# Kernel tuning notes

Hardware: AMD Instinct MI355X
Metric: run time of the kernel (lower is better)

## Reference

```python
import jax, jax.numpy as jnp
import numpy as np


def setup_inputs() -> dict:
    key0 = jax.random.key(0)
    kq, kk, kv = jax.random.split(key0, 3)
    B, S, E = 4, 2048, 1024
    query = jax.random.normal(kq, (B, S, E), dtype=jnp.float32)
    key = jax.random.normal(kk, (B, S, E), dtype=jnp.float32)
    value = jax.random.normal(kv, (B, S, E), dtype=jnp.float32)
    attn_mask = jnp.zeros((B, S, S), dtype=jnp.float32)
    return {"query": query, "key": key, "value": value, "attn_mask": attn_mask}


def reference(query, key, value, attn_mask):
    # qk = Q K^T / sqrt(E) + mask; softmax over last dim; dropout is
    # identity in eval mode (reference baseline); out = attn @ V.
    E = query.shape[-1]
    scale = 1.0 / jnp.sqrt(jnp.asarray(E, dtype=query.dtype))
    qk = jnp.einsum("bqe,bke->bqk", query, key) * scale + attn_mask
    attn = jax.nn.softmax(qk, axis=-1)
    out = jnp.einsum("bqk,bke->bqe", attn, value)
    return out
```

## Files before the change

### kernel.cpp

```cpp
#include <hip/hip_runtime.h>
#include <stdint.h>
#include <math.h>

typedef unsigned short u16;
typedef short bf16x8 __attribute__((ext_vector_type(8)));
typedef unsigned short u16x8 __attribute__((ext_vector_type(8)));
typedef unsigned short u16x4 __attribute__((ext_vector_type(4)));
typedef float f32x4 __attribute__((ext_vector_type(4)));

typedef __attribute__((address_space(1))) const void gvoid;
typedef __attribute__((address_space(3))) void lvoid;

#define LOG2E 1.4426950408889634f

__device__ __forceinline__ float bf2f(u16 u) {
  union { unsigned int i; float f; } v; v.i = ((unsigned int)u) << 16; return v.f;
}
__device__ __forceinline__ u16 f2bf(float f) {
  union { float ff; unsigned int i; } v; v.ff = f;
  unsigned int x = v.i;
  return (u16)((x + 0x7FFFu + ((x >> 16) & 1u)) >> 16);
}

__global__ __launch_bounds__(256)
void cvt2_f32_bf16(const float* __restrict__ s0, u16* __restrict__ d0,
                   const float* __restrict__ s1, u16* __restrict__ d1, long n)
{
  const long nb = n / 2048;
  const float* src = (blockIdx.x < nb) ? s0 : s1;
  u16* dst         = (blockIdx.x < nb) ? d0 : d1;
  const long bid   = (blockIdx.x < nb) ? blockIdx.x : (blockIdx.x - nb);
  long i = (bid * 256 + threadIdx.x) * 8;
  if (i + 8 > n) return;
  f32x4 a = *(const f32x4*)&src[i];
  f32x4 b = *(const f32x4*)&src[i + 4];
  u16x8 o;
#pragma unroll
  for (int j = 0; j < 4; j++) { o[j] = f2bf(a[j]); o[4 + j] = f2bf(b[j]); }
  *(u16x8*)&dst[i] = o;
}

__global__ __launch_bounds__(256)
void cvt_f32_bf16(const float* __restrict__ src, u16* __restrict__ dst, long n)
{
  long i = ((long)blockIdx.x * 256 + threadIdx.x) * 8;
  if (i + 8 > n) return;
  f32x4 a = *(const f32x4*)&src[i];
  f32x4 b = *(const f32x4*)&src[i + 4];
  u16x8 o;
#pragma unroll
  for (int j = 0; j < 4; j++) { o[j] = f2bf(a[j]); o[4 + j] = f2bf(b[j]); }
  *(u16x8*)&dst[i] = o;
}

__global__ __launch_bounds__(256)
void transcvt_v(const float* __restrict__ V, u16* __restrict__ VT, int S, int E)
{
  __shared__ u16 t[64][72];
  const int b = blockIdx.z;
  const float* Vb = V + (long)b * S * E;
  u16* VTb = VT + (long)b * S * E;
  const int k0 = blockIdx.x * 64, n0 = blockIdx.y * 64;
  const int tid = threadIdx.x;
#pragma unroll
  for (int p = 0; p < 2; p++) {
    int kk = p * 32 + (tid >> 3);
    int nn = (tid & 7) * 8;
    f32x4 a = *(const f32x4*)&Vb[(long)(k0 + kk) * E + n0 + nn];
    f32x4 c = *(const f32x4*)&Vb[(long)(k0 + kk) * E + n0 + nn + 4];
#pragma unroll
    for (int j = 0; j < 4; j++) { t[nn + j][kk] = f2bf(a[j]); t[nn + 4 + j][kk] = f2bf(c[j]); }
  }
  __syncthreads();
#pragma unroll
  for (int p = 0; p < 2; p++) {
    int nn = p * 32 + (tid >> 3);
    int kk = (tid & 7) * 8;
    u16x8 u;
#pragma unroll
    for (int j = 0; j < 8; j++) u[j] = t[nn][kk + j];
    *(u16x8*)&VTb[(long)(n0 + nn) * S + k0 + kk] = u;
  }
}

__global__ __launch_bounds__(512, 1)
void gemm_bt_256(const u16* __restrict__ A, int lda,
                 const u16* __restrict__ B, int ldb, long bBatchStride,
                 u16* __restrict__ C, int ldc,
                 int K, float scale, int S)
{
  __shared__ u16 LA[2][256][64];
  __shared__ u16 LB[2][256][64];

  const int tid  = threadIdx.x;
  const int lane = tid & 63;
  const int wave = tid >> 6;
  const int wm   = wave >> 2;
  const int wn   = wave & 3;
  const long gTile = (long)blockIdx.y * 256;
  const int  bidx  = (int)(gTile / S);
  const int  nTile = blockIdx.x * 256;

  const u16* Ab = A + gTile * (long)lda;
  const u16* Bb = B + (long)bidx * bBatchStride + (long)nTile * ldb;

  const int lm  = lane & 15;
  const int lkc = (lane >> 4) * 8;
  const int srw = lane >> 3;
  const int scg = (lane & 7) * 8;

  f32x4 acc[8][4];
#pragma unroll
  for (int i = 0; i < 8; i++)
#pragma unroll
    for (int j = 0; j < 4; j++) acc[i][j] = (f32x4){0.f, 0.f, 0.f, 0.f};

  bf16x8 afr[8], bA[4], bB[4];

#define STG_A(buf, T, h)                                                      \
  {                                                                           \
    _Pragma("unroll")                                                         \
    for (int p_ = 0; p_ < 2; p_++) {                                          \
      const int ch_ = wave * 2 + p_;                                          \
      const int rr_ = (h) * 128 + ch_ * 8 + srw;                              \
      __builtin_amdgcn_global_load_lds(                                       \
          (gvoid*)&Ab[(long)rr_ * lda + (T) * 64 + scg],                      \
          (lvoid*)((char*)&LA[0][0][0] + (buf) * 32768 + (h) * 16384 + ch_ * 1024), \
          16, 0, 0);                                                          \
    }                                                                         \
  }
#define STG_B(buf, T, h)                                                      \
  {                                                                           \
    _Pragma("unroll")                                                         \
    for (int p_ = 0; p_ < 2; p_++) {                                          \
      const int ch_ = wave * 2 + p_;                                          \
      const int rr_ = (h) * 128 + ch_ * 8 + srw;                              \
      __builtin_amdgcn_global_load_lds(                                       \
          (gvoid*)&Bb[(long)rr_ * ldb + (T) * 64 + scg],                      \
          (lvoid*)((char*)&LB[0][0][0] + (buf) * 32768 + (h) * 16384 + ch_ * 1024), \
          16, 0, 0);                                                          \
    }                                                                         \
  }

#define LDA_HALF(buf, mh)                                                     \
  {                                                                           \
    _Pragma("unroll")                                                         \
    for (int m_ = 0; m_ < 4; m_++)                                            \
      _Pragma("unroll")                                                       \
      for (int kk_ = 0; kk_ < 2; kk_++)                                       \
        afr[m_ * 2 + kk_] = *(const bf16x8*)&LA[buf][wm * 128 + ((mh) * 4 + m_) * 16 + lm][kk_ * 32 + lkc]; \
  }
#define LDB_HALF(buf, nh, dst)                                                \
  {                                                                           \
    _Pragma("unroll")                                                         \
    for (int n_ = 0; n_ < 2; n_++)                                            \
      _Pragma("unroll")                                                       \
      for (int kk_ = 0; kk_ < 2; kk_++)                                       \
        dst[n_ * 2 + kk_] = *(const bf16x8*)&LB[buf][wn * 64 + ((nh) * 2 + n_) * 16 + lm][kk_ * 32 + lkc]; \
  }

#define PH(mh, nh, bp)                                                        \
  {                                                                           \
    __builtin_amdgcn_sched_barrier(0);                                        \
    __builtin_amdgcn_s_barrier();                                             \
    asm volatile("s_waitcnt lgkmcnt(0)" ::: "memory");                        \
    __builtin_amdgcn_sched_barrier(0);                                        \
    __builtin_amdgcn_s_setprio(1);                                            \
    _Pragma("unroll")                                                         \
    for (int m_ = 0; m_ < 4; m_++)                                            \
      _Pragma("unroll")                                                       \
      for (int n_ = 0; n_ < 2; n_++)                                          \
        _Pragma("unroll")                                                     \
        for (int kk_ = 0; kk_ < 2; kk_++)                                     \
          acc[(mh) * 4 + m_][(nh) * 2 + n_] =                                 \
              __builtin_amdgcn_mfma_f32_16x16x32_bf16(                        \
                  afr[m_ * 2 + kk_], bp[n_ * 2 + kk_],                        \
                  acc[(mh) * 4 + m_][(nh) * 2 + n_], 0, 0, 0);                \
    __builtin_amdgcn_s_setprio(0);                                            \
    __builtin_amdgcn_sched_barrier(0);                                        \
    __builtin_amdgcn_s_barrier();                                             \
  }

  const int NT = K >> 6;
  const int NI = NT >> 1;

  STG_A(0, 0, 0); STG_A(0, 0, 1); STG_B(0, 0, 0); STG_B(0, 0, 1);
  STG_A(1, 1, 0); STG_B(1, 1, 0);
  asm volatile("s_waitcnt vmcnt(0)" ::: "memory");
  __builtin_amdgcn_sched_barrier(0);
  __builtin_amdgcn_s_barrier();

  for (int i = 0; i < NI - 1; i++) {
    const int t0 = 2 * i, t1 = t0 + 1;
    LDA_HALF(0, 0); LDB_HALF(0, 0, bA);
    STG_B(1, t1, 1);
    PH(0, 0, bA);
    LDB_HALF(0, 1, bB);
    STG_A(1, t1, 1);
    PH(0, 1, bB);
    LDA_HALF(0, 1);
    STG_A(0, t0 + 2, 0);
    PH(1, 0, bA);
    STG_B(0, t0 + 2, 0);
    asm volatile("s_waitcnt vmcnt(4)" ::: "memory");
    PH(1, 1, bB);
    LDA_HALF(1, 0); LDB_HALF(1, 0, bA);
    STG_B(0, t0 + 2, 1);
    PH(0, 0, bA);
    LDB_HALF(1, 1, bB);
    STG_A(0, t0 + 2, 1);
    PH(0, 1, bB);
    LDA_HALF(1, 1);
    STG_A(1, t1 + 2, 0);
    PH(1, 0, bA);
    STG_B(1, t1 + 2, 0);
    asm volatile("s_waitcnt vmcnt(4)" ::: "memory");
    PH(1, 1, bB);
  }

  {
    const int t1 = NT - 1;
    LDA_HALF(0, 0); LDB_HALF(0, 0, bA);
    STG_B(1, t1, 1);
    PH(0, 0, bA);
    LDB_HALF(0, 1, bB);
    STG_A(1, t1, 1);
    PH(0, 1, bB);
    LDA_HALF(0, 1);
    PH(1, 0, bA);
    asm volatile("s_waitcnt vmcnt(0)" ::: "memory");
    PH(1, 1, bB);
    LDA_HALF(1, 0); LDB_HALF(1, 0, bA);
    PH(0, 0, bA);
    LDB_HALF(1, 1, bB);
    PH(0, 1, bB);
    LDA_HALF(1, 1);
    PH(1, 0, bA);
    PH(1, 1, bB);
  }

  const int lr = (lane >> 4) * 4;
#pragma unroll
  for (int mf = 0; mf < 8; mf++) {
#pragma unroll
    for (int nf = 0; nf < 4; nf++) {
      long gr = gTile + wm * 128 + mf * 16 + lr;
      int  cc = nTile + wn * 64 + nf * 16 + lm;
#pragma unroll
      for (int i2 = 0; i2 < 4; i2++)
        C[(gr + i2) * (long)ldc + cc] = f2bf(acc[mf][nf][i2] * scale);
    }
  }
#undef STG_A
#undef STG_B
#undef LDA_HALF
#undef LDB_HALF
#undef PH
}

template<int HASMASK, int COUT>
__global__ __launch_bounds__(256, 3)
void gemm_bt_fast(const u16* __restrict__ A, int lda, long aRowOff,
                  const u16* __restrict__ B, int ldb, long bBatchStride,
                  void* __restrict__ Cp, int ldc, long cRowOff,
                  const float* __restrict__ maskf,
                  int K, float scale, long g0, int S)
{
  const int tid  = threadIdx.x;
  const int lane = tid & 63;
  const int wave = tid >> 6;
  const long gTile = g0 + (long)blockIdx.y * 128;
  const int  bidx  = (int)(gTile / S);
  const int  nTile = blockIdx.x * 128;

  __shared__ u16 As[128][32];
  __shared__ u16 Bs[128][32];

  const u16* Ab = A + (gTile - aRowOff) * (long)lda;
  const u16* Bb = B + (long)bidx * bBatchStride + (long)nTile * ldb;

  const int qm = (wave >> 1) * 64;
  const int qn = (wave & 1) * 64;
  const int lm  = lane & 15;
  const int lkB = (lane >> 4) * 16;

  const int sr = lane >> 2;
  const int sc = (lane & 3) * 8;

  f32x4 acc[4][4];
#pragma unroll
  for (int i = 0; i < 4; i++)
#pragma unroll
    for (int j = 0; j < 4; j++) acc[i][j] = (f32x4){0.f, 0.f, 0.f, 0.f};

  for (int k0 = 0; k0 < K; k0 += 32) {
#pragma unroll
    for (int p = 0; p < 2; p++) {
      const int chunk = wave * 2 + p;
      const int r = chunk * 16 + sr;
      __builtin_amdgcn_global_load_lds(
          (gvoid*)&Ab[(long)r * lda + k0 + sc],
          (lvoid*)((char*)&As[0][0] + chunk * 1024),
          16, 0, 0);
      __builtin_amdgcn_global_load_lds(
          (gvoid*)&Bb[(long)r * ldb + k0 + sc],
          (lvoid*)((char*)&Bs[0][0] + chunk * 1024),
          16, 0, 0);
    }
    __syncthreads();

    bf16x8 af[4], bfr[4];
#pragma unroll
    for (int rt = 0; rt < 4; rt++)
      af[rt] = *(const bf16x8*)((const char*)&As[qm + rt * 16 + lm][0] + lkB);
#pragma unroll
    for (int ct = 0; ct < 4; ct++)
      bfr[ct] = *(const bf16x8*)((const char*)&Bs[qn + ct * 16 + lm][0] + lkB);

#pragma unroll
    for (int rt = 0; rt < 4; rt++)
#pragma unroll
      for (int ct = 0; ct < 4; ct++)
        acc[rt][ct] = __builtin_amdgcn_mfma_f32_16x16x32_bf16(af[rt], bfr[ct], acc[rt][ct], 0, 0, 0);
    __syncthreads();
  }

  const int lr = (lane >> 4) * 4;
#pragma unroll
  for (int rt = 0; rt < 4; rt++) {
#pragma unroll
    for (int ct = 0; ct < 4; ct++) {
      long gr = gTile + qm + rt * 16 + lr;
      int  cc = nTile + qn + ct * 16 + lm;
#pragma unroll
      for (int i = 0; i < 4; i++) {
        float v = acc[rt][ct][i] * scale;
        if (HASMASK) v += maskf[(gr + i) * (long)ldc + cc];
        if (COUT == 0)
          ((u16*)Cp)[(gr + i - cRowOff) * (long)ldc + cc] = f2bf(v);
        else
          ((float*)Cp)[(gr + i - cRowOff) * (long)ldc + cc] = v;
      }
    }
  }
}

template<int ASRC, int BSRC, int BMODE, int HASMASK, int COUT>
__global__ __launch_bounds__(256, 2)
void gemm_bt(const void* __restrict__ Ap, int lda, long aRowOff,
             const void* __restrict__ Bp, int ldb, long bBatchStride,
             void* __restrict__ Cp, int ldc, long cRowOff,
             const float* __restrict__ maskf,
             int K, float scale, long g0, int S)
{
  const int tid  = threadIdx.x;
  const int lane = tid & 63;
  const int wave = tid >> 6;
  const long gTile = g0 + (long)blockIdx.y * 128;
  const int  b     = (int)(gTile / S);
  const int  nTile = blockIdx.x * 128;

  __shared__ u16 As[128][40];
  __shared__ u16 Bs[128][40];

  const int qm = (wave >> 1) * 64;
  const int qn = (wave & 1) * 64;

  f32x4 acc[4][4];
#pragma unroll
  for (int i = 0; i < 4; i++)
#pragma unroll
    for (int j = 0; j < 4; j++) acc[i][j] = (f32x4){0.f, 0.f, 0.f, 0.f};

  const u16*   Ab = (const u16*)Ap   + (gTile - aRowOff) * (long)lda;
  const float* Af = (const float*)Ap + (gTile - aRowOff) * (long)lda;
  const u16*   Bb = (const u16*)Bp   + (long)b * bBatchStride;
  const float* Bf = (const float*)Bp + (long)b * bBatchStride;

  const int lm = lane & 15;
  const int lk = (lane >> 4) * 8;

  for (int k0 = 0; k0 < K; k0 += 32) {
    if (ASRC == 0) {
      int srow = tid >> 2, scol = (tid & 3) * 8;
#pragma unroll
      for (int p = 0; p < 2; p++) {
        int r = p * 64 + srow;
        *(u16x8*)&As[r][scol] = *(const u16x8*)&Ab[(long)r * lda + k0 + scol];
      }
    } else {
      int srow = tid >> 3, scol = (tid & 7) * 4;
#pragma unroll
      for (int p = 0; p < 4; p++) {
        int r = p * 32 + srow;
        f32x4 a = *(const f32x4*)&Af[(long)r * lda + k0 + scol];
        u16x4 o;
#pragma unroll
        for (int j = 0; j < 4; j++) o[j] = f2bf(a[j]);
        *(u16x4*)&As[r][scol] = o;
      }
    }
    if (BMODE == 0) {
      if (BSRC == 0) {
        int srow = tid >> 2, scol = (tid & 3) * 8;
#pragma unroll
        for (int p = 0; p < 2; p++) {
          int r = p * 64 + srow;
          *(u16x8*)&Bs[r][scol] = *(const u16x8*)&Bb[(long)(nTile + r) * ldb + k0 + scol];
        }
      } else {
        int srow = tid >> 3, scol = (tid & 7) * 4;
#pragma unroll
        for (int p = 0; p < 4; p++) {
          int r = p * 32 + srow;
          f32x4 a = *(const f32x4*)&Bf[(long)(nTile + r) * ldb + k0 + scol];
          u16x4 o;
#pragma unroll
          for (int j = 0; j < 4; j++) o[j] = f2bf(a[j]);
          *(u16x4*)&Bs[r][scol] = o;
        }
      }
    }
    __syncthreads();

    bf16x8 af[4], bfr[4];
#pragma unroll
    for (int rt = 0; rt < 4; rt++)
      af[rt] = *(const bf16x8*)&As[qm + rt * 16 + lm][lk];
    if (BMODE == 0) {
#pragma unroll
      for (int ct = 0; ct < 4; ct++)
        bfr[ct] = *(const bf16x8*)&Bs[qn + ct * 16 + lm][lk];
    } else {
#pragma unroll
      for (int ct = 0; ct < 4; ct++) {
        const float* vp = Bf + (long)(k0 + lk) * ldb + nTile + qn + ct * 16 + lm;
#pragma unroll
        for (int j = 0; j < 8; j++) bfr[ct][j] = (short)f2bf(vp[(long)j * ldb]);
      }
    }
#pragma unroll
    for (int rt = 0; rt < 4; rt++)
#pragma unroll
      for (int ct = 0; ct < 4; ct++)
        acc[rt][ct] = __builtin_amdgcn_mfma_f32_16x16x32_bf16(af[rt], bfr[ct], acc[rt][ct], 0, 0, 0);
    __syncthreads();
  }

  const int lr = (lane >> 4) * 4;
#pragma unroll
  for (int rt = 0; rt < 4; rt++) {
#pragma unroll
    for (int ct = 0; ct < 4; ct++) {
      long gr = gTile + qm + rt * 16 + lr;
      int  cc = nTile + qn + ct * 16 + lm;
#pragma unroll
      for (int i = 0; i < 4; i++) {
        float v = acc[rt][ct][i] * scale;
        if (HASMASK) v += maskf[(gr + i) * (long)ldc + cc];
        if (COUT == 0)
          ((u16*)Cp)[(gr + i - cRowOff) * (long)ldc + cc] = f2bf(v);
        else
          ((float*)Cp)[(gr + i - cRowOff) * (long)ldc + cc] = v;
      }
    }
  }
}

template<int HASM>
__global__ __launch_bounds__(256)
void softmax_rows(u16* __restrict__ Sbuf, const float* __restrict__ maskf, int ncols)
{
  const long row = blockIdx.x;
  u16* rp = Sbuf + row * (long)ncols;
  const int tid = threadIdx.x;

  u16x8 u = *(const u16x8*)&rp[tid * 8];
  float x[8];
  if (HASM) {
    const float* mp = maskf + row * (long)ncols + tid * 8;
    f32x4 ma = *(const f32x4*)&mp[0];
    f32x4 mb = *(const f32x4*)&mp[4];
#pragma unroll
    for (int i = 0; i < 4; i++) { x[i] = bf2f(u[i]) + ma[i]; x[4 + i] = bf2f(u[4 + i]) + mb[i]; }
  } else {
#pragma unroll
    for (int i = 0; i < 8; i++) x[i] = bf2f(u[i]);
  }
  float m = -3.0e38f;
#pragma unroll
  for (int i = 0; i < 8; i++) m = fmaxf(m, x[i]);
#pragma unroll
  for (int off = 32; off; off >>= 1) m = fmaxf(m, __shfl_xor(m, off, 64));
  __shared__ float redm[4];
  if ((tid & 63) == 0) redm[tid >> 6] = m;
  __syncthreads();
  m = fmaxf(fmaxf(redm[0], redm[1]), fmaxf(redm[2], redm[3]));

  float e[8];
  float s = 0.f;
#pragma unroll
  for (int i = 0; i < 8; i++) { e[i] = exp2f((x[i] - m) * LOG2E); s += e[i]; }
#pragma unroll
  for (int off = 32; off; off >>= 1) s += __shfl_xor(s, off, 64);
  __shared__ float reds[4];
  if ((tid & 63) == 0) reds[tid >> 6] = s;
  __syncthreads();
  s = reds[0] + reds[1] + reds[2] + reds[3];

  float inv = 1.0f / s;
  u16x8 o;
#pragma unroll
  for (int i = 0; i < 8; i++) o[i] = f2bf(e[i] * inv);
  *(u16x8*)&rp[tid * 8] = o;
}

extern "C" void kernel_launch(void* const* d_in, const int* in_sizes, int n_in,
                              void* d_out, int out_size, void* d_ws, size_t ws_size,
                              hipStream_t stream)
{
  const float* Q    = (const float*)d_in[0];
  const float* Km   = (const float*)d_in[1];
  const float* V    = (const float*)d_in[2];
  const float* mask = (const float*)d_in[3];
  float* out = (float*)d_out;

  const long qsz = in_sizes[0];
  const long msz = in_sizes[3];
  const long E = 1024;
  const long S = (msz / qsz) * E;
  const long B = qsz / (S * E);
  const long G = B * S;
  const float scale = 1.0f / sqrtf((float)E);

  const size_t mergedBytes = (size_t)(2 * qsz) * 2 + (size_t)G * S * 2;
  if (ws_size >= mergedBytes && (S % 256) == 0 && (G % 256) == 0) {
    char* w = (char*)d_ws;
    u16* Qb   = (u16*)w;
    u16* Kb   = (u16*)(w + (size_t)qsz * 2);
    u16* Sbuf = (u16*)(w + (size_t)(2 * qsz) * 2);
    u16* VTb  = Qb;

    cvt2_f32_bf16<<<dim3((unsigned)(2 * qsz / 2048)), 256, 0, stream>>>(
        Q, Qb, Km, Kb, qsz);

    gemm_bt_256<<<dim3(S / 256, G / 256), 512, 0, stream>>>(
        Qb, (int)E, Kb, (int)E, S * E,
        Sbuf, (int)S, (int)E, scale, (int)S);

    softmax_rows<1><<<dim3((unsigned)G), 256, 0, stream>>>(Sbuf, mask, (int)S);

    transcvt_v<<<dim3(S / 64, E / 64, B), 256, 0, stream>>>(V, VTb, (int)S, (int)E);

    gemm_bt_fast<0, 1><<<dim3(E / 128, G / 128), 256, 0, stream>>>(
        Sbuf, (int)S, 0L, VTb, (int)S, E * S,
        out, (int)E, 0L, nullptr, (int)S, 1.0f, 0L, (int)S);
    return;
  }

  const size_t convBytes = (size_t)(3 * qsz) * 2;
  const size_t rowBytes  = (size_t)S * 2;
  char* w = (char*)d_ws;
  size_t avail = ws_size;
  const bool haveConv = (ws_size >= convBytes + 128 * rowBytes);

  u16 *Qb = nullptr, *Kb = nullptr, *VTb = nullptr;
  if (haveConv) {
    Qb  = (u16*)w;              w += (size_t)qsz * 2;
    Kb  = (u16*)w;              w += (size_t)qsz * 2;
    VTb = (u16*)w;              w += (size_t)qsz * 2;
    avail -= convBytes;
  }
  long Rmax = (long)((avail / rowBytes) / 128) * 128;
  if (Rmax > G) Rmax = G;
  if (Rmax < 128) Rmax = 128;
  u16* Sbuf = (u16*)w;

  if (haveConv) {
    cvt_f32_bf16<<<dim3((unsigned)(qsz / 2048)), 256, 0, stream>>>(Q, Qb, qsz);
    cvt_f32_bf16<<<dim3((unsigned)(qsz / 2048)), 256, 0, stream>>>(Km, Kb, qsz);
    transcvt_v<<<dim3(S / 64, E / 64, B), 256, 0, stream>>>(V, VTb, (int)S, (int)E);
  }

  for (long g0 = 0; g0 < G; g0 += Rmax) {
    const long R = (G - g0 < Rmax) ? (G - g0) : Rmax;
    if (haveConv) {
      gemm_bt_fast<1, 0><<<dim3(S / 128, R / 128), 256, 0, stream>>>(
          Qb, (int)E, 0L, Kb, (int)E, S * E,
          Sbuf, (int)S, g0, mask, (int)E, scale, g0, (int)S);
    } else {
      gemm_bt<1, 1, 0, 1, 0><<<dim3(S / 128, R / 128), 256, 0, stream>>>(
          Q, (int)E, 0L, Km, (int)E, S * E,
          Sbuf, (int)S, g0, mask, (int)E, scale, g0, (int)S);
    }
    softmax_rows<0><<<dim3(R), 256, 0, stream>>>(Sbuf, nullptr, (int)S);
    if (haveConv) {
      gemm_bt_fast<0, 1><<<dim3(E / 128, R / 128), 256, 0, stream>>>(
          Sbuf, (int)S, g0, VTb, (int)S, E * S,
          out, (int)E, 0L, nullptr, (int)S, 1.0f, g0, (int)S);
    } else {
      gemm_bt<0, 1, 1, 0, 1><<<dim3(E / 128, R / 128), 256, 0, stream>>>(
          Sbuf, (int)S, g0, V, (int)E, S * E,
          out, (int)E, 0L, nullptr, (int)S, 1.0f, g0, (int)S);
    }
  }
}
```

Measured before the change: 286.1 us.

## Swizzle LDS layout in 256 GEMM and use wave-per-row softmax

Applies an XOR swizzle to the 16-byte column chunks when staging A/B tiles into LDS and when reading fragments, to cut LDS bank conflicts in the QK^T GEMM. It also replaces the block-per-row softmax with a kernel where each wave handles one 2048-wide row, using shuffle reductions so no LDS or block barriers are needed. The fast path now requires S divisible by 512, and the new softmax assumes ncols equals 2048.

Result: faster. 277.6 us (-3.0%).

```diff
diff --git a/kernel.cpp b/kernel.cpp
--- a/kernel.cpp
+++ b/kernel.cpp
@@ -105,9 +105,10 @@
   const u16* Bb = B + (long)bidx * bBatchStride + (long)nTile * ldb;
 
   const int lm  = lane & 15;
-  const int lkc = (lane >> 4) * 8;
+  const int lmx = lm & 7;
+  const int l47 = lane >> 4;
   const int srw = lane >> 3;
-  const int scg = (lane & 7) * 8;
+  const int scg = (((lane & 7) ^ (lane >> 3)) * 8);
 
   f32x4 acc[8][4];
 #pragma unroll
@@ -148,7 +149,7 @@
     for (int m_ = 0; m_ < 4; m_++)                                            \
       _Pragma("unroll")                                                       \
       for (int kk_ = 0; kk_ < 2; kk_++)                                       \
-        afr[m_ * 2 + kk_] = *(const bf16x8*)&LA[buf][wm * 128 + ((mh) * 4 + m_) * 16 + lm][kk_ * 32 + lkc]; \
+        afr[m_ * 2 + kk_] = *(const bf16x8*)&LA[buf][wm * 128 + ((mh) * 4 + m_) * 16 + lm][(((kk_ * 4 + l47) ^ lmx) * 8)]; \
   }
 #define LDB_HALF(buf, nh, dst)                                                \
   {                                                                           \
@@ -156,7 +157,7 @@
     for (int n_ = 0; n_ < 2; n_++)                                            \
       _Pragma("unroll")                                                       \
       for (int kk_ = 0; kk_ < 2; kk_++)                                       \
-        dst[n_ * 2 + kk_] = *(const bf16x8*)&LB[buf][wn * 64 + ((nh) * 2 + n_) * 16 + lm][kk_ * 32 + lkc]; \
+        dst[n_ * 2 + kk_] = *(const bf16x8*)&LB[buf][wn * 64 + ((nh) * 2 + n_) * 16 + lm][(((kk_ * 4 + l47) ^ lmx) * 8)]; \
   }
 
 #define PH(mh, nh, bp)                                                        \
@@ -467,6 +468,52 @@
   }
 }
 
+__global__ __launch_bounds__(256)
+void softmax_rows_wave(u16* __restrict__ Sbuf, const float* __restrict__ maskf,
+                       int ncols)
+{
+  const int wave = threadIdx.x >> 6;
+  const int lane = threadIdx.x & 63;
+  const long row = (long)blockIdx.x * 4 + wave;
+  u16* rp = Sbuf + row * (long)ncols;
+  const float* mp = maskf + row * (long)ncols;
+
+  float x[32];
+  float m = -3.0e38f;
+#pragma unroll
+  for (int j = 0; j < 4; j++) {
+    const int c = j * 512 + lane * 8;
+    u16x8 u = *(const u16x8*)&rp[c];
+    f32x4 ma = *(const f32x4*)&mp[c];
+    f32x4 mb = *(const f32x4*)&mp[c + 4];
+#pragma unroll
+    for (int i = 0; i < 4; i++) {
+      x[j * 8 + i]     = bf2f(u[i])     + ma[i];
+      x[j * 8 + 4 + i] = bf2f(u[4 + i]) + mb[i];
+    }
+#pragma unroll
+    for (int i = 0; i < 8; i++) m = fmaxf(m, x[j * 8 + i]);
+  }
+#pragma unroll
+  for (int off = 32; off; off >>= 1) m = fmaxf(m, __shfl_xor(m, off, 64));
+
+  float s = 0.f;
+#pragma unroll
+  for (int i = 0; i < 32; i++) { x[i] = exp2f((x[i] - m) * LOG2E); s += x[i]; }
+#pragma unroll
+  for (int off = 32; off; off >>= 1) s += __shfl_xor(s, off, 64);
+  const float inv = 1.0f / s;
+
+#pragma unroll
+  for (int j = 0; j < 4; j++) {
+    const int c = j * 512 + lane * 8;
+    u16x8 o;
+#pragma unroll
+    for (int i = 0; i < 8; i++) o[i] = f2bf(x[j * 8 + i] * inv);
+    *(u16x8*)&rp[c] = o;
+  }
+}
+
 template<int HASM>
 __global__ __launch_bounds__(256)
 void softmax_rows(u16* __restrict__ Sbuf, const float* __restrict__ maskf, int ncols)
@@ -534,7 +581,7 @@
   const float scale = 1.0f / sqrtf((float)E);
 
   const size_t mergedBytes = (size_t)(2 * qsz) * 2 + (size_t)G * S * 2;
-  if (ws_size >= mergedBytes && (S % 256) == 0 && (G % 256) == 0) {
+  if (ws_size >= mergedBytes && (S % 512) == 0 && (G % 256) == 0) {
     char* w = (char*)d_ws;
     u16* Qb   = (u16*)w;
     u16* Kb   = (u16*)(w + (size_t)qsz * 2);
@@ -548,7 +595,8 @@
         Qb, (int)E, Kb, (int)E, S * E,
         Sbuf, (int)S, (int)E, scale, (int)S);
 
-    softmax_rows<1><<<dim3((unsigned)G), 256, 0, stream>>>(Sbuf, mask, (int)S);
+    softmax_rows_wave<<<dim3((unsigned)(G / 4)), 256, 0, stream>>>(
+        Sbuf, mask, (int)S);
 
     transcvt_v<<<dim3(S / 64, E / 64, B), 256, 0, stream>>>(V, VTb, (int)S, (int)E);
 
```
